# Performance work log

Hardware: AMD Instinct MI355X
Metric: run time of the kernel (lower is better)

The kernel has to match this reference:

```python
import jax, jax.numpy as jnp
import numpy as np

N_NODES = 100000


def gcn_conv(x, W, b, src, dst, n):
    # PyG GCNConv: linear transform, add self-loops, symmetric degree normalization,
    # scatter-add aggregation from src -> dst, then bias.
    h = x @ W  # [N, F_out]
    loop = jnp.arange(n, dtype=src.dtype)
    s = jnp.concatenate([src, loop])  # sources incl. self-loops
    d = jnp.concatenate([dst, loop])  # targets incl. self-loops
    deg = jax.ops.segment_sum(jnp.ones_like(d, dtype=h.dtype), d, num_segments=n)
    dinv = jnp.where(deg > 0, jax.lax.rsqrt(deg), 0.0)
    norm = dinv[s] * dinv[d]  # [E+N]
    msg = h[s] * norm[:, None]  # gather + scale
    out = jax.ops.segment_sum(msg, d, num_segments=n)  # scatter-add
    return out + b


def setup_inputs() -> dict:
    key = jax.random.key(0)
    k1, k2, k3, k4 = jax.random.split(key, 4)
    n, e = N_NODES, 1600000
    z = jax.random.normal(k1, (n, 64), dtype=jnp.float32)
    edge_index = jax.random.randint(k2, (2, e), 0, n, dtype=jnp.int64)
    # Glorot-ish init for weights, zero bias (PyG default bias init is zeros)
    W1 = jax.random.normal(k3, (64, 128), dtype=jnp.float32) * (1.0 / np.sqrt(64))
    b1 = jnp.zeros((128,), dtype=jnp.float32)
    W2 = jax.random.normal(k4, (128, 64), dtype=jnp.float32) * (1.0 / np.sqrt(128))
    b2 = jnp.zeros((64,), dtype=jnp.float32)
    return {"z": z, "edge_index": edge_index, "W1": W1, "b1": b1, "W2": W2, "b2": b2}


def reference(z, edge_index, W1, b1, W2, b2):
    n = z.shape[0]
    src, dst = edge_index[0], edge_index[1]
    h = gcn_conv(z, W1, b1, src, dst, n)
    h = jax.nn.relu(h)
    x_hat = gcn_conv(h, W2, b2, src, dst, n)
    return x_hat
```

## Files before the change

kernel.cpp:

```cpp
#include <hip/hip_runtime.h>
#include <hip/hip_bf16.h>


#define WAVE 64
#define BSHIFT 8
#define NPB 256
#define CAP 5120
#define CH 4096
#define NBMAX 512

typedef __attribute__((ext_vector_type(8))) short bf16x8;
typedef __attribute__((ext_vector_type(4))) float f32x4;

__device__ inline float bf16_to_f32(unsigned short h) {
    return __uint_as_float(((unsigned int)h) << 16);
}
__device__ inline unsigned short f32_to_bf16(float f) {
    unsigned int x = __float_as_uint(f);
    return (unsigned short)((x + 0x7FFFu + ((x >> 16) & 1u)) >> 16);
}

__global__ void prep(const float* __restrict__ W1, const float* __restrict__ W2,
                     unsigned short* __restrict__ W1t, unsigned short* __restrict__ W2t,
                     int* __restrict__ bcursor, int NB)
{
    int i = blockIdx.x * blockDim.x + threadIdx.x;
    if (i < NB) bcursor[i] = 0;
    if (i < 128 * 64) {
        int n = i >> 6, k = i & 63;
        W1t[i] = f32_to_bf16(W1[k * 128 + n]);
    }
    if (i < 64 * 128) {
        int n = i >> 7, k = i & 127;
        W2t[i] = f32_to_bf16(W2[k * 64 + n]);
    }
}

__global__ __launch_bounds__(256) void bin_edges(
        const int* __restrict__ src, const int* __restrict__ dst,
        int* __restrict__ bcursor, int2* __restrict__ ebuf, int E, int NB)
{
    __shared__ int hist[NBMAX];
    __shared__ int cur[NBMAX];
    const int t  = threadIdx.x;
    const int e0 = blockIdx.x * CH;

    for (int b = t; b < NB; b += 256) hist[b] = 0;
    __syncthreads();

#pragma unroll
    for (int j = 0; j < CH / 256; ++j) {
        int e = e0 + j * 256 + t;
        if (e < E) atomicAdd(&hist[dst[e] >> BSHIFT], 1);
    }
    __syncthreads();

    for (int b = t; b < NB; b += 256) {
        int c = hist[b];
        cur[b] = (c > 0) ? atomicAdd(&bcursor[b], c) : 0;
    }
    __syncthreads();

#pragma unroll
    for (int j = 0; j < CH / 256; ++j) {
        int e = e0 + j * 256 + t;
        if (e < E) {
            int s = src[e], d = dst[e];
            int b = d >> BSHIFT;
            int pos = atomicAdd(&cur[b], 1);
            ebuf[(size_t)b * CAP + pos] = make_int2(s, d);
        }
    }
}

__global__ __launch_bounds__(256) void build_csr(
        const int2* __restrict__ ebuf, const int* __restrict__ bcursor,
        const float* __restrict__ z, float* __restrict__ dinv,
        int* __restrict__ rbeg, int* __restrict__ rend,
        int* __restrict__ csr, unsigned short* __restrict__ u, int N)
{
    __shared__ int   h[NPB];
    __shared__ int   tmp[NPB];
    __shared__ float sdv[NPB];
    const int t   = threadIdx.x;
    const int b   = blockIdx.x;
    const int n0  = b << BSHIFT;
    const int cnt = bcursor[b];
    const size_t base = (size_t)b * CAP;

    h[t] = 0;
    __syncthreads();

    for (int i = t; i < cnt; i += 256)
        atomicAdd(&h[ebuf[base + i].y - n0], 1);
    __syncthreads();

    int deg = h[t];
    tmp[t] = deg;
    __syncthreads();
    for (int off = 1; off < 256; off <<= 1) {
        int x = (t >= off) ? tmp[t - off] : 0;
        __syncthreads();
        tmp[t] += x;
        __syncthreads();
    }
    int st = tmp[t] - deg;

    int node = n0 + t;
    float di = rsqrtf((float)deg + 1.0f);
    sdv[t] = di;
    if (node < N) {
        dinv[node] = di;
        rbeg[node] = (int)base + st;
        rend[node] = (int)base + st + deg;
    }
    h[t] = st;
    __syncthreads();

    for (int i = t; i < cnt; i += 256) {
        int2 e = ebuf[base + i];
        int p = atomicAdd(&h[e.y - n0], 1);
        csr[base + p] = e.x;
    }

    const int nloc = (N - n0 < NPB) ? (N - n0) : NPB;
    for (int i = t; i < nloc * 16; i += 256) {
        int r = i >> 4, kq = i & 15;
        float d2 = sdv[r];
        float4 v = ((const float4*)(z + (size_t)(n0 + r) * 64))[kq];
        ushort4 o;
        o.x = f32_to_bf16(v.x * d2);
        o.y = f32_to_bf16(v.y * d2);
        o.z = f32_to_bf16(v.z * d2);
        o.w = f32_to_bf16(v.w * d2);
        ((ushort4*)(u + (size_t)(n0 + r) * 64))[kq] = o;
    }
}

template<bool POST>
__global__ __launch_bounds__(256) void aggregate64_bf16(
        const unsigned short* __restrict__ hs, const int* __restrict__ rbeg,
        const int* __restrict__ rend, const int* __restrict__ csr,
        const float* __restrict__ dinv, const float* __restrict__ b,
        void* __restrict__ out_, int N)
{
    int node = (int)((blockIdx.x * (size_t)blockDim.x + threadIdx.x) >> 6);
    int lane = threadIdx.x & 63;
    if (node >= N) return;
    node = __builtin_amdgcn_readfirstlane(node);

    const int beg = rbeg[node];
    const int end = rend[node];

    float acc = bf16_to_f32(hs[(size_t)node * 64 + lane]);

    int e = beg;
    for (; e + 16 <= end; e += 16) {
        int s[16];
#pragma unroll
        for (int j = 0; j < 16; ++j) s[j] = csr[e + j];
        float v[16];
#pragma unroll
        for (int j = 0; j < 16; ++j) v[j] = bf16_to_f32(hs[(size_t)s[j] * 64 + lane]);
        float t0 = ((v[0] + v[1]) + (v[2] + v[3])) + ((v[4] + v[5]) + (v[6] + v[7]));
        float t1 = ((v[8] + v[9]) + (v[10] + v[11])) + ((v[12] + v[13]) + (v[14] + v[15]));
        acc += t0 + t1;
    }
    for (; e + 4 <= end; e += 4) {
        int s0 = csr[e+0], s1 = csr[e+1], s2 = csr[e+2], s3 = csr[e+3];
        float v0 = bf16_to_f32(hs[(size_t)s0 * 64 + lane]);
        float v1 = bf16_to_f32(hs[(size_t)s1 * 64 + lane]);
        float v2 = bf16_to_f32(hs[(size_t)s2 * 64 + lane]);
        float v3 = bf16_to_f32(hs[(size_t)s3 * 64 + lane]);
        acc += (v0 + v1) + (v2 + v3);
    }
    for (; e < end; ++e)
        acc += bf16_to_f32(hs[(size_t)csr[e] * 64 + lane]);

    if (POST) {
        float o = dinv[node] * acc + b[lane];
        ((float*)out_)[(size_t)node * 64 + lane] = o;
    } else {
        ((unsigned short*)out_)[(size_t)node * 64 + lane] = f32_to_bf16(acc);
    }
}

#define TILE 32
#define W1T_ST 72
#define W2T_ST 136
#define A_ST   72
#define X1_ST  136

__global__ __launch_bounds__(256) void gemm12_mfma(
        const unsigned short* __restrict__ agg1,
        const unsigned short* __restrict__ W1t,
        const float* __restrict__ b1,
        const unsigned short* __restrict__ W2t,
        const float* __restrict__ dinv,
        unsigned short* __restrict__ hs2, int N)
{
    __shared__ unsigned short sW1[128 * W1T_ST];
    __shared__ unsigned short sW2[64 * W2T_ST];
    __shared__ unsigned short sA[TILE * A_ST];
    __shared__ unsigned short sX[TILE * X1_ST];
    __shared__ float sdv[TILE];

    const int tid  = threadIdx.x;
    const int row0 = blockIdx.x * TILE;
    const int lane = tid & 63;
    const int wv   = tid >> 6;
    const int l16  = lane & 15;
    const int quad = lane >> 4;

    for (int i = tid; i < 128 * 8; i += 256) {
        int r = i >> 3, c = i & 7;
        *(uint4*)&sW1[r * W1T_ST + c * 8] = *(const uint4*)&W1t[r * 64 + c * 8];
    }
    for (int i = tid; i < 64 * 16; i += 256) {
        int r = i >> 4, c = i & 15;
        *(uint4*)&sW2[r * W2T_ST + c * 8] = *(const uint4*)&W2t[r * 128 + c * 8];
    }
    for (int i = tid; i < TILE * 8; i += 256) {
        int r = i >> 3, c = i & 7;
        int gr = row0 + r;
        uint4 v = make_uint4(0u, 0u, 0u, 0u);
        if (gr < N) v = *(const uint4*)&agg1[(size_t)gr * 64 + c * 8];
        *(uint4*)&sA[r * A_ST + c * 8] = v;
    }
    if (tid < TILE) {
        int gr = row0 + tid;
        sdv[tid] = (gr < N) ? dinv[gr] : 0.0f;
    }
    __syncthreads();

    {
        const int mt  = wv & 1;
        const int ntb = (wv >> 1) * 4;
        f32x4 acc[4];
#pragma unroll
        for (int t = 0; t < 4; ++t) acc[t] = (f32x4)0.0f;

#pragma unroll
        for (int k0 = 0; k0 < 64; k0 += 32) {
            bf16x8 af = *(const bf16x8*)&sA[(mt * 16 + l16) * A_ST + k0 + quad * 8];
#pragma unroll
            for (int t = 0; t < 4; ++t) {
                bf16x8 bf = *(const bf16x8*)&sW1[((ntb + t) * 16 + l16) * W1T_ST + k0 + quad * 8];
                acc[t] = __builtin_amdgcn_mfma_f32_16x16x32_bf16(af, bf, acc[t], 0, 0, 0);
            }
        }

#pragma unroll
        for (int t = 0; t < 4; ++t) {
            int col = (ntb + t) * 16 + l16;
            float bb = b1[col];
#pragma unroll
            for (int r = 0; r < 4; ++r) {
                int lr = mt * 16 + quad * 4 + r;
                float o = fmaxf(acc[t][r] * sdv[lr] + bb, 0.0f);
                sX[lr * X1_ST + col] = f32_to_bf16(o);
            }
        }
    }
    __syncthreads();

    {
        const int mt  = wv & 1;
        const int ntb = (wv >> 1) * 2;
        f32x4 acc[2];
#pragma unroll
        for (int t = 0; t < 2; ++t) acc[t] = (f32x4)0.0f;

#pragma unroll
        for (int k0 = 0; k0 < 128; k0 += 32) {
            bf16x8 af = *(const bf16x8*)&sX[(mt * 16 + l16) * X1_ST + k0 + quad * 8];
#pragma unroll
            for (int t = 0; t < 2; ++t) {
                bf16x8 bf = *(const bf16x8*)&sW2[((ntb + t) * 16 + l16) * W2T_ST + k0 + quad * 8];
                acc[t] = __builtin_amdgcn_mfma_f32_16x16x32_bf16(af, bf, acc[t], 0, 0, 0);
            }
        }

#pragma unroll
        for (int t = 0; t < 2; ++t) {
            int col = (ntb + t) * 16 + l16;
#pragma unroll
            for (int r = 0; r < 4; ++r) {
                int lr = mt * 16 + quad * 4 + r;
                int gr = row0 + lr;
                if (gr < N)
                    hs2[(size_t)gr * 64 + col] = f32_to_bf16(acc[t][r] * sdv[lr]);
            }
        }
    }
}

static inline size_t align_up(size_t x, size_t a) { return (x + a - 1) / a * a; }

extern "C" void kernel_launch(void* const* d_in, const int* in_sizes, int n_in,
                              void* d_out, int out_size, void* d_ws, size_t ws_size,
                              hipStream_t stream) {
    const float* z    = (const float*)d_in[0];
    const int*   eidx = (const int*)d_in[1];
    const float* W1   = (const float*)d_in[2];
    const float* b1   = (const float*)d_in[3];
    const float* W2   = (const float*)d_in[4];
    const float* b2   = (const float*)d_in[5];
    float* out = (float*)d_out;

    const int N = in_sizes[0] / 64;
    const int E = in_sizes[1] / 2;
    const int* src = eidx;
    const int* dst = eidx + E;
    const int NB = (N + NPB - 1) >> BSHIFT;

    char* ws = (char*)d_ws;
    size_t off = 0;
    float* dinv    = (float*)(ws + off); off = align_up(off + (size_t)N * 4, 512);
    int*   rbeg    = (int*)  (ws + off); off = align_up(off + (size_t)N * 4, 512);
    int*   rend    = (int*)  (ws + off); off = align_up(off + (size_t)N * 4, 512);
    int*   bcursor = (int*)  (ws + off); off = align_up(off + (size_t)NBMAX * 4, 512);
    unsigned short* W1t = (unsigned short*)(ws + off); off = align_up(off + 8192 * 2, 512);
    unsigned short* W2t = (unsigned short*)(ws + off); off = align_up(off + 8192 * 2, 512);
    int*   csr     = (int*)  (ws + off); off = align_up(off + (size_t)NB * CAP * 4, 512);
    float* bufA    = (float*)(ws + off); off = align_up(off + (size_t)N * 64 * 4, 512);
    float* bufB    = (float*)(ws + off); off = align_up(off + (size_t)N * 64 * 4, 512);
    float* bufC    = (float*)(ws + off); off = align_up(off + (size_t)N * 128 * 4, 512);
    int2*  ebuf    = (int2*)bufC;
    (void)ws_size;

    unsigned short* u    = (unsigned short*)bufA;
    unsigned short* agg1 = (unsigned short*)bufB;
    unsigned short* hs2  = (unsigned short*)bufA;

    prep<<<32, 256, 0, stream>>>(W1, W2, W1t, W2t, bcursor, NB);

    bin_edges<<<(E + CH - 1) / CH, 256, 0, stream>>>(src, dst, bcursor, ebuf, E, NB);
    build_csr<<<NB, 256, 0, stream>>>(ebuf, bcursor, z, dinv, rbeg, rend, csr, u, N);

    aggregate64_bf16<false><<<(N + 3) / 4, 256, 0, stream>>>(u, rbeg, rend, csr, dinv, nullptr, agg1, N);

    gemm12_mfma<<<(N + TILE - 1) / TILE, 256, 0, stream>>>(agg1, W1t, b1, W2t, dinv, hs2, N);

    aggregate64_bf16<true><<<(N + 3) / 4, 256, 0, stream>>>(hs2, rbeg, rend, csr, dinv, b2, out, N);
}
```

Measured before the change: 241.9 us.

## Split edge buffer into src ints and byte-local dst, widen gather batch, add nontemporal hints

The binned edge buffer changes from int2 (src,dst) to a separate int src array plus a one-byte local destination index, which cuts traffic in the binning and CSR build passes. The aggregation loop now uses one 32-wide masked gather with a tree reduction in place of the 16/4/1 tail loops. This issues more loads in flight, but it wastes gathers on padded lanes for low-degree nodes and uses more registers. Nontemporal loads and stores are added for streaming reads of src, esrc and z and for the final output write.

After: 336.4 us. +39.1%, slower.

```diff
diff --git a/kernel.cpp b/kernel.cpp
--- a/kernel.cpp
+++ b/kernel.cpp
@@ -20,6 +20,36 @@
     return (unsigned short)((x + 0x7FFFu + ((x >> 16) & 1u)) >> 16);
 }
 
+__device__ inline float gather_rows32(const unsigned short* __restrict__ hs,
+                                      const int* __restrict__ csr,
+                                      int beg, int end, int lane, float acc)
+{
+    const int last = end - 1;
+    for (int e = beg; e < end; e += 32) {
+        int s[32];
+#pragma unroll
+        for (int j = 0; j < 32; ++j) {
+            int idx = e + j;
+            s[j] = csr[idx < end ? idx : last];
+        }
+        float v[32];
+#pragma unroll
+        for (int j = 0; j < 32; ++j)
+            v[j] = bf16_to_f32(hs[(size_t)s[j] * 64 + lane]);
+#pragma unroll
+        for (int j = 0; j < 32; ++j)
+            v[j] = (e + j < end) ? v[j] : 0.0f;
+#pragma unroll
+        for (int w = 16; w >= 1; w >>= 1)
+#pragma unroll
+            for (int j = 0; j < 32; ++j) {
+                if (j < w) v[j] = v[2 * j] + v[2 * j + 1];
+            }
+        acc += v[0];
+    }
+    return acc;
+}
+
 __global__ void prep(const float* __restrict__ W1, const float* __restrict__ W2,
                      unsigned short* __restrict__ W1t, unsigned short* __restrict__ W2t,
                      int* __restrict__ bcursor, int NB)
@@ -38,7 +68,8 @@
 
 __global__ __launch_bounds__(256) void bin_edges(
         const int* __restrict__ src, const int* __restrict__ dst,
-        int* __restrict__ bcursor, int2* __restrict__ ebuf, int E, int NB)
+        int* __restrict__ bcursor, int* __restrict__ esrc,
+        unsigned char* __restrict__ edloc, int E, int NB)
 {
     __shared__ int hist[NBMAX];
     __shared__ int cur[NBMAX];
@@ -65,16 +96,20 @@
     for (int j = 0; j < CH / 256; ++j) {
         int e = e0 + j * 256 + t;
         if (e < E) {
-            int s = src[e], d = dst[e];
+            int s = __builtin_nontemporal_load(&src[e]);
+            int d = dst[e];
             int b = d >> BSHIFT;
             int pos = atomicAdd(&cur[b], 1);
-            ebuf[(size_t)b * CAP + pos] = make_int2(s, d);
+            size_t idx = (size_t)b * CAP + pos;
+            esrc[idx]  = s;
+            edloc[idx] = (unsigned char)(d & (NPB - 1));
         }
     }
 }
 
 __global__ __launch_bounds__(256) void build_csr(
-        const int2* __restrict__ ebuf, const int* __restrict__ bcursor,
+        const int* __restrict__ esrc, const unsigned char* __restrict__ edloc,
+        const int* __restrict__ bcursor,
         const float* __restrict__ z, float* __restrict__ dinv,
         int* __restrict__ rbeg, int* __restrict__ rend,
         int* __restrict__ csr, unsigned short* __restrict__ u, int N)
@@ -92,7 +127,7 @@
     __syncthreads();
 
     for (int i = t; i < cnt; i += 256)
-        atomicAdd(&h[ebuf[base + i].y - n0], 1);
+        atomicAdd(&h[edloc[base + i]], 1);
     __syncthreads();
 
     int deg = h[t];
@@ -118,21 +153,22 @@
     __syncthreads();
 
     for (int i = t; i < cnt; i += 256) {
-        int2 e = ebuf[base + i];
-        int p = atomicAdd(&h[e.y - n0], 1);
-        csr[base + p] = e.x;
+        int dl = edloc[base + i];
+        int p = atomicAdd(&h[dl], 1);
+        csr[base + p] = __builtin_nontemporal_load(&esrc[base + i]);
     }
 
     const int nloc = (N - n0 < NPB) ? (N - n0) : NPB;
     for (int i = t; i < nloc * 16; i += 256) {
         int r = i >> 4, kq = i & 15;
         float d2 = sdv[r];
-        float4 v = ((const float4*)(z + (size_t)(n0 + r) * 64))[kq];
+        const f32x4* zr = (const f32x4*)(z + (size_t)(n0 + r) * 64);
+        f32x4 v = __builtin_nontemporal_load(zr + kq);
         ushort4 o;
-        o.x = f32_to_bf16(v.x * d2);
-        o.y = f32_to_bf16(v.y * d2);
-        o.z = f32_to_bf16(v.z * d2);
-        o.w = f32_to_bf16(v.w * d2);
+        o.x = f32_to_bf16(v[0] * d2);
+        o.y = f32_to_bf16(v[1] * d2);
+        o.z = f32_to_bf16(v[2] * d2);
+        o.w = f32_to_bf16(v[3] * d2);
         ((ushort4*)(u + (size_t)(n0 + r) * 64))[kq] = o;
     }
 }
@@ -153,33 +189,11 @@
     const int end = rend[node];
 
     float acc = bf16_to_f32(hs[(size_t)node * 64 + lane]);
-
-    int e = beg;
-    for (; e + 16 <= end; e += 16) {
-        int s[16];
-#pragma unroll
-        for (int j = 0; j < 16; ++j) s[j] = csr[e + j];
-        float v[16];
-#pragma unroll
-        for (int j = 0; j < 16; ++j) v[j] = bf16_to_f32(hs[(size_t)s[j] * 64 + lane]);
-        float t0 = ((v[0] + v[1]) + (v[2] + v[3])) + ((v[4] + v[5]) + (v[6] + v[7]));
-        float t1 = ((v[8] + v[9]) + (v[10] + v[11])) + ((v[12] + v[13]) + (v[14] + v[15]));
-        acc += t0 + t1;
-    }
-    for (; e + 4 <= end; e += 4) {
-        int s0 = csr[e+0], s1 = csr[e+1], s2 = csr[e+2], s3 = csr[e+3];
-        float v0 = bf16_to_f32(hs[(size_t)s0 * 64 + lane]);
-        float v1 = bf16_to_f32(hs[(size_t)s1 * 64 + lane]);
-        float v2 = bf16_to_f32(hs[(size_t)s2 * 64 + lane]);
-        float v3 = bf16_to_f32(hs[(size_t)s3 * 64 + lane]);
-        acc += (v0 + v1) + (v2 + v3);
-    }
-    for (; e < end; ++e)
-        acc += bf16_to_f32(hs[(size_t)csr[e] * 64 + lane]);
+    acc = gather_rows32(hs, csr, beg, end, lane, acc);
 
     if (POST) {
         float o = dinv[node] * acc + b[lane];
-        ((float*)out_)[(size_t)node * 64 + lane] = o;
+        __builtin_nontemporal_store(o, &((float*)out_)[(size_t)node * 64 + lane]);
     } else {
         ((unsigned short*)out_)[(size_t)node * 64 + lane] = f32_to_bf16(acc);
     }
@@ -326,17 +340,18 @@
     float* bufA    = (float*)(ws + off); off = align_up(off + (size_t)N * 64 * 4, 512);
     float* bufB    = (float*)(ws + off); off = align_up(off + (size_t)N * 64 * 4, 512);
     float* bufC    = (float*)(ws + off); off = align_up(off + (size_t)N * 128 * 4, 512);
-    int2*  ebuf    = (int2*)bufC;
     (void)ws_size;
 
     unsigned short* u    = (unsigned short*)bufA;
     unsigned short* agg1 = (unsigned short*)bufB;
     unsigned short* hs2  = (unsigned short*)bufA;
+    int*            esrc  = (int*)bufC;
+    unsigned char*  edloc = (unsigned char*)((char*)bufC + (size_t)NB * CAP * 4);
 
     prep<<<32, 256, 0, stream>>>(W1, W2, W1t, W2t, bcursor, NB);
 
-    bin_edges<<<(E + CH - 1) / CH, 256, 0, stream>>>(src, dst, bcursor, ebuf, E, NB);
-    build_csr<<<NB, 256, 0, stream>>>(ebuf, bcursor, z, dinv, rbeg, rend, csr, u, N);
+    bin_edges<<<(E + CH - 1) / CH, 256, 0, stream>>>(src, dst, bcursor, esrc, edloc, E, NB);
+    build_csr<<<NB, 256, 0, stream>>>(esrc, edloc, bcursor, z, dinv, rbeg, rend, csr, u, N);
 
     aggregate64_bf16<false><<<(N + 3) / 4, 256, 0, stream>>>(u, rbeg, rend, csr, dinv, nullptr, agg1, N);
 
```
